# Optimization experiments

Measured on AMD Instinct MI355X. Metric: run time of the kernel, lower is better.

Reference implementation:

```python
import jax, jax.numpy as jnp
import numpy as np

NUM_COMPONENTS = 4
HEADS = 24
DIM_HEAD = 64
EPS = 1e-8

def setup_inputs() -> dict:
    key = jax.random.key(0)
    ks = jax.random.split(key, 6)
    BC, S, D = 8, 4096, 1536   # batch*components, spatial tokens, hidden dim
    T = 154                     # encoder (text) sequence length
    w_scale = D ** -0.5
    return {
        "hidden_states": jax.random.normal(ks[0], (BC, S, D), jnp.float32),
        "encoder_hidden_states": jax.random.normal(ks[1], (BC, T, D), jnp.float32),
        "Wq": jax.random.normal(ks[2], (D, D), jnp.float32) * w_scale,
        "bq": jnp.zeros((D,), jnp.float32),
        "Wk": jax.random.normal(ks[3], (D, D), jnp.float32) * w_scale,
        "bk": jnp.zeros((D,), jnp.float32),
        "Wv": jax.random.normal(ks[4], (D, D), jnp.float32) * w_scale,
        "bv": jnp.zeros((D,), jnp.float32),
        "Wo": jax.random.normal(ks[5], (D, D), jnp.float32) * w_scale,
        "bo": jnp.zeros((D,), jnp.float32),
    }

def reference(hidden_states, encoder_hidden_states, Wq, bq, Wk, bk, Wv, bv, Wo, bo):
    BC, S, D = hidden_states.shape
    T = encoder_hidden_states.shape[1]
    C = NUM_COMPONENTS
    B = BC // C
    H, dh = HEADS, DIM_HEAD
    scale = dh ** -0.5

    # linear projections (torch Linear: x @ W.T + b)
    q = hidden_states @ Wq.T + bq            # [BC, S, D]
    k = encoder_hidden_states @ Wk.T + bk     # [BC, T, D]
    v = encoder_hidden_states @ Wv.T + bv     # [BC, T, D]

    q = q.reshape(BC, S, H, dh).transpose(0, 2, 1, 3)  # [BC, H, S, dh]
    k = k.reshape(BC, T, H, dh).transpose(0, 2, 1, 3)  # [BC, H, T, dh]
    v = v.reshape(BC, T, H, dh).transpose(0, 2, 1, 3)  # [BC, H, T, dh]

    # full score tensor, softmax over the COMPONENT axis, then renormalize over keys
    scores = jnp.einsum('bhsd,bhtd->bhst', q, k) * scale        # [BC, H, S, T]
    scores = scores.reshape(C, B, H, S, T)
    w = jax.nn.softmax(scores, axis=0).reshape(BC, H, S, T)
    w = w / (jnp.sum(w, axis=-1, keepdims=True) + EPS)

    out = jnp.einsum('bhst,bhtd->bhsd', w, v)                   # [BC, H, S, dh]
    out = out.transpose(0, 2, 1, 3).reshape(BC, S, D)
    out = out @ Wo.T + bo
    return out
```

## Files before the change

### kernel.cpp

```cpp
#include <hip/hip_runtime.h>


typedef unsigned short u16;
typedef unsigned int   u32;

#define NHS   50331648ULL
#define NEHS  1892352ULL
#define NW    2359296ULL
#define NVT   1966080ULL

using bf16x8 = __attribute__((ext_vector_type(8))) short;
using f32x4  = __attribute__((ext_vector_type(4))) float;

__device__ __forceinline__ u16 f2bf(float f) {
  union { float f; u32 u; } x{f};
  u32 r = (x.u + 0x7fffu + ((x.u >> 16) & 1u)) >> 16;
  return (u16)r;
}

__device__ __forceinline__ void gload_lds16(const u16* g, u16* s) {
  __builtin_amdgcn_global_load_lds((const __attribute__((address_space(1))) void*)g,
                                   (__attribute__((address_space(3))) void*)s,
                                   16, 0, 0);
}

#define WAITV(N) asm volatile("s_waitcnt vmcnt(" #N ")" ::: "memory")

__global__ void cvt_bf16(const float* __restrict__ src, u16* __restrict__ dst, int n4) {
  int idx = blockIdx.x * blockDim.x + threadIdx.x;
  int stride = gridDim.x * blockDim.x;
  for (int i = idx; i < n4; i += stride) {
    float4 v = ((const float4*)src)[i];
    ushort4 o;
    o.x = f2bf(v.x); o.y = f2bf(v.y); o.z = f2bf(v.z); o.w = f2bf(v.w);
    ((ushort4*)dst)[i] = o;
  }
}

template <int MODE>
__global__ __launch_bounds__(512, 2)
void gemm_big(const u16* __restrict__ Ag, const u16* __restrict__ Bw,
              const float* __restrict__ bias, void* __restrict__ Cv) {
  __shared__ __align__(16) u16 lds[65536];

  const int tid  = threadIdx.x;
  const int wv   = tid >> 6;
  const int lane = tid & 63;
  const int l16  = lane & 15, quad = lane >> 4;
  const int wm = wv >> 2, wn = wv & 3;

  const int wg = ((int)blockIdx.x & 7) * 96 + ((int)blockIdx.x >> 3);
  const int by = wg & 127;
  const int bx = wg >> 7;
  const int m0 = by * 256, n0 = bx * 256;

  const u16* gsrc[4];
  int ldst[4];
#pragma unroll
  for (int q = 0; q < 4; ++q) {
    const int L = q * 512 + tid;
    const int cid = L & 1023;
    const int row = cid >> 2;
    const int csrc = ((L & 3) ^ ((row >> 1) & 3)) * 8;
    gsrc[q] = (L < 1024 ? Ag + (size_t)(m0 + row) * 1536
                        : Bw + (size_t)(n0 + row) * 1536) + csrc;
    ldst[q] = L * 8;
  }

  int aoff[8], boff[4];
#pragma unroll
  for (int i = 0; i < 8; ++i) {
    const int ra = wm * 128 + i * 16 + l16;
    aoff[i] = ra * 32 + ((quad ^ ((ra >> 1) & 3)) * 8);
  }
#pragma unroll
  for (int j = 0; j < 4; ++j) {
    const int rb = wn * 64 + j * 16 + l16;
    boff[j] = 8192 + rb * 32 + ((quad ^ ((rb >> 1) & 3)) * 8);
  }

  f32x4 acc[8][4];
#pragma unroll
  for (int i = 0; i < 8; ++i)
#pragma unroll
    for (int j = 0; j < 4; ++j) acc[i][j] = {0.f, 0.f, 0.f, 0.f};

  auto stage2 = [&](int tile, int qb) {
    u16* dst = &lds[(tile & 3) * 16384];
    const int kt = tile * 32;
    gload_lds16(gsrc[qb] + kt, dst + ldst[qb]);
    gload_lds16(gsrc[qb + 1] + kt, dst + ldst[qb + 1]);
  };

#define TILE_BODY(T, DO_STAGE, WAITCODE)                                      \
  {                                                                           \
    const u16* buf = &lds[((T) & 3) * 16384];                                 \
    bf16x8 bfr[4], af[4];                                                     \
    _Pragma("unroll") for (int j = 0; j < 4; ++j)                             \
      bfr[j] = *(const bf16x8*)&buf[boff[j]];                                 \
    _Pragma("unroll") for (int i = 0; i < 4; ++i)                             \
      af[i] = *(const bf16x8*)&buf[aoff[i]];                                  \
    if (DO_STAGE) stage2((T) + 3, 0);                                         \
    __builtin_amdgcn_s_barrier();                                             \
    __builtin_amdgcn_s_setprio(1);                                            \
    _Pragma("unroll") for (int i = 0; i < 4; ++i)                             \
      _Pragma("unroll") for (int j = 0; j < 4; ++j)                           \
        acc[i][j] = __builtin_amdgcn_mfma_f32_16x16x32_bf16(af[i], bfr[j],    \
                                                            acc[i][j], 0, 0, 0); \
    __builtin_amdgcn_s_setprio(0);                                            \
    __builtin_amdgcn_s_barrier();                                             \
    _Pragma("unroll") for (int i = 0; i < 4; ++i)                             \
      af[i] = *(const bf16x8*)&buf[aoff[4 + i]];                              \
    if (DO_STAGE) stage2((T) + 3, 2);                                         \
    __builtin_amdgcn_s_barrier();                                             \
    __builtin_amdgcn_s_setprio(1);                                            \
    _Pragma("unroll") for (int i = 0; i < 4; ++i)                             \
      _Pragma("unroll") for (int j = 0; j < 4; ++j)                           \
        acc[4 + i][j] = __builtin_amdgcn_mfma_f32_16x16x32_bf16(af[i], bfr[j],\
                                                        acc[4 + i][j], 0, 0, 0); \
    __builtin_amdgcn_s_setprio(0);                                            \
    WAITCODE;                                                                 \
    __builtin_amdgcn_s_barrier();                                             \
  }

  stage2(0, 0); stage2(0, 2);
  stage2(1, 0); stage2(1, 2);
  stage2(2, 0); stage2(2, 2);
  WAITV(8);
  __builtin_amdgcn_s_barrier();

  for (int t = 0; t < 45; ++t)
    TILE_BODY(t, true, WAITV(8));
  TILE_BODY(45, false, WAITV(4));
  TILE_BODY(46, false, WAITV(0));
  TILE_BODY(47, false, (void)0);
#undef TILE_BODY

#pragma unroll
  for (int i = 0; i < 8; ++i) {
    const int row0 = m0 + wm * 128 + i * 16 + quad * 4;
#pragma unroll
    for (int j = 0; j < 4; ++j) {
      const int col = n0 + wn * 64 + j * 16 + l16;
      const float bvs = bias[col];
#pragma unroll
      for (int rr = 0; rr < 4; ++rr) {
        const int row = row0 + rr;
        const float v = acc[i][j][rr] + bvs;
        if (MODE == 0) ((float*)Cv)[(size_t)row * 1536 + col] = v;
        else           ((u16*)Cv)[(size_t)row * 1536 + col] = f2bf(v);
      }
    }
  }
}

template <int MODE>
__global__ __launch_bounds__(256)
void gemm_bt(const u16* __restrict__ A, const u16* __restrict__ Bw,
             const float* __restrict__ bias, void* __restrict__ Cv,
             int M, int K) {
  const int N = 1536;
  __shared__ __align__(16) u16 As[4096];
  __shared__ __align__(16) u16 Bs[4096];
  const int tid  = threadIdx.x;
  const int wv   = tid >> 6;
  const int lane = tid & 63;
  const int wr = wv >> 1, wc = wv & 1;
  const int l16 = lane & 15, quad = lane >> 4;
  const int m0 = blockIdx.y * 128, n0 = blockIdx.x * 128;
  const int r = tid >> 2, c8 = (tid & 3) * 8;

  int ra0 = m0 + r;      if (ra0 > M - 1) ra0 = M - 1;
  int ra1 = m0 + 64 + r; if (ra1 > M - 1) ra1 = M - 1;
  const u16* a0 = A  + (size_t)ra0 * K + c8;
  const u16* a1 = A  + (size_t)ra1 * K + c8;
  const u16* b0 = Bw + (size_t)(n0 + r) * K + c8;
  const u16* b1 = Bw + (size_t)(n0 + 64 + r) * K + c8;
  u16* asd0 = &As[tid * 8];
  u16* asd1 = &As[2048 + tid * 8];
  u16* bsd0 = &Bs[tid * 8];
  u16* bsd1 = &Bs[2048 + tid * 8];

  f32x4 acc[4][4];
#pragma unroll
  for (int i = 0; i < 4; ++i)
#pragma unroll
    for (int j = 0; j < 4; ++j) acc[i][j] = {0.f, 0.f, 0.f, 0.f};

  for (int kt = 0; kt < K; kt += 32) {
    __syncthreads();
    gload_lds16(a0 + kt, asd0);
    gload_lds16(a1 + kt, asd1);
    gload_lds16(b0 + kt, bsd0);
    gload_lds16(b1 + kt, bsd1);
    __syncthreads();
    bf16x8 af[4], bfr[4];
#pragma unroll
    for (int i = 0; i < 4; ++i) {
      af[i]  = *(const bf16x8*)&As[(wr * 64 + i * 16 + l16) * 32 + quad * 8];
      bfr[i] = *(const bf16x8*)&Bs[(wc * 64 + i * 16 + l16) * 32 + quad * 8];
    }
#pragma unroll
    for (int i = 0; i < 4; ++i)
#pragma unroll
      for (int j = 0; j < 4; ++j)
        acc[i][j] = __builtin_amdgcn_mfma_f32_16x16x32_bf16(af[i], bfr[j], acc[i][j], 0, 0, 0);
  }

#pragma unroll
  for (int i = 0; i < 4; ++i) {
    const int rb = m0 + wr * 64 + i * 16 + quad * 4;
#pragma unroll
    for (int j = 0; j < 4; ++j) {
      const int col = n0 + wc * 64 + j * 16 + l16;
      const float bvs = bias[col];
#pragma unroll
      for (int rr = 0; rr < 4; ++rr) {
        const int row = rb + rr;
        if (row < M) {
          float v = acc[i][j][rr] + bvs;
          if (MODE == 1) {
            ((u16*)Cv)[(size_t)row * N + col] = f2bf(v);
          } else {
            const int bc = row / 154;
            const int t  = row - bc * 154;
            ((u16*)Cv)[((size_t)bc * 1536 + col) * 160 + t] = f2bf(v);
          }
        }
      }
    }
  }
}

__global__ __launch_bounds__(256, 2)
void attn_kernel(const u16* __restrict__ qg, const u16* __restrict__ kg,
                 const u16* __restrict__ vtg, u16* __restrict__ og) {
  __shared__ __align__(16) u16 lds[40960];

  const int tid  = threadIdx.x;
  const int wv   = tid >> 6;
  const int lane = tid & 63;
  const int l16 = lane & 15, quad = lane >> 4;
  const int s0 = blockIdx.x * 64;
  const int h  = blockIdx.y;
  const int b  = blockIdx.z;
  const int swz = ((quad ^ ((l16 >> 1) & 3)) * 8);

  {
    const u16* kbase = kg + (size_t)b * 154 * 1536 + h * 64;
#pragma unroll
    for (int p = 0; p < 20; ++p) {
      const int L = p * 256 + tid;
      const int r = L >> 2;
      const int t = r % 160;
      const int cks = r / 160;
      const int c = cks >> 1, ks = cks & 1;
      const int csrc = ((L & 3) ^ ((t >> 1) & 3)) * 8;
      const u16* src = kbase + ((size_t)c * 308 + t) * 1536 + ks * 32 + csrc;
      gload_lds16(src, &lds[(size_t)L * 8]);
    }
  }

  bf16x8 qa[4][2];
#pragma unroll
  for (int c = 0; c < 4; ++c) {
    const u16* qrow = qg + ((size_t)((c * 2 + b) * 4096 + s0 + wv * 16 + l16)) * 1536 + h * 64;
#pragma unroll
    for (int ks = 0; ks < 2; ++ks)
      qa[c][ks] = *(const bf16x8*)(qrow + ks * 32 + quad * 8);
  }
  __syncthreads();

  f32x4 sc[4][10];
#pragma unroll
  for (int c = 0; c < 4; ++c)
#pragma unroll
    for (int nt = 0; nt < 10; ++nt) sc[c][nt] = {0.f, 0.f, 0.f, 0.f};

#pragma unroll
  for (int nt = 0; nt < 10; ++nt)
#pragma unroll
    for (int c = 0; c < 4; ++c)
#pragma unroll
      for (int ks = 0; ks < 2; ++ks) {
        bf16x8 kf = *(const bf16x8*)&lds[((c * 2 + ks) * 160 + nt * 16 + l16) * 32 + swz];
        sc[c][nt] = __builtin_amdgcn_mfma_f32_16x16x32_bf16(qa[c][ks], kf, sc[c][nt], 0, 0, 0);
      }

  float rs[4][4];
#pragma unroll
  for (int c = 0; c < 4; ++c)
#pragma unroll
    for (int rr = 0; rr < 4; ++rr) rs[c][rr] = 0.f;

#pragma unroll
  for (int nt = 0; nt < 10; ++nt) {
    const int t = nt * 16 + l16;
    const bool ok = (t < 154);
#pragma unroll
    for (int rr = 0; rr < 4; ++rr) {
      float v0 = sc[0][nt][rr] * 0.125f;
      float v1 = sc[1][nt][rr] * 0.125f;
      float v2 = sc[2][nt][rr] * 0.125f;
      float v3 = sc[3][nt][rr] * 0.125f;
      float m = fmaxf(fmaxf(v0, v1), fmaxf(v2, v3));
      float e0 = __expf(v0 - m), e1 = __expf(v1 - m);
      float e2 = __expf(v2 - m), e3 = __expf(v3 - m);
      float inv = 1.f / (e0 + e1 + e2 + e3);
      float w0 = ok ? e0 * inv : 0.f;
      float w1 = ok ? e1 * inv : 0.f;
      float w2 = ok ? e2 * inv : 0.f;
      float w3 = ok ? e3 * inv : 0.f;
      sc[0][nt][rr] = w0; sc[1][nt][rr] = w1; sc[2][nt][rr] = w2; sc[3][nt][rr] = w3;
      rs[0][rr] += w0; rs[1][rr] += w1; rs[2][rr] += w2; rs[3][rr] += w3;
    }
  }
#pragma unroll
  for (int c = 0; c < 4; ++c)
#pragma unroll
    for (int rr = 0; rr < 4; ++rr) {
      float v = rs[c][rr];
      v += __shfl_xor(v, 1); v += __shfl_xor(v, 2);
      v += __shfl_xor(v, 4); v += __shfl_xor(v, 8);
      rs[c][rr] = 1.f / (v + 1e-8f);
    }

  __syncthreads();

  const u16* vbase = vtg + ((size_t)b * 1536 + h * 64) * 160;

  auto stage_v = [&](int c, int par) {
    const u16* vb = vbase + (size_t)c * 2 * 1536 * 160;
    u16* slot = &lds[20480 + par * 10240];
#pragma unroll
    for (int p = 0; p < 5; ++p) {
      const int L = p * 256 + tid;
      const int row = L >> 2;
      const int ks = row >> 6, dh = row & 63;
      const int csrc = ((L & 3) ^ ((dh >> 1) & 3)) * 8;
      gload_lds16(vb + dh * 160 + ks * 32 + csrc, &slot[(size_t)L * 8]);
    }
  };

  auto write_w = [&](int c, int par) {
    u16* slot = &lds[par * 10240];
#pragma unroll
    for (int nt = 0; nt < 10; ++nt) {
#pragma unroll
      for (int rr = 0; rr < 4; ++rr) {
        const int srow = wv * 16 + quad * 4 + rr;
        const int t = nt * 16 + l16;
        const int cl = ((t >> 3) & 3) ^ ((srow >> 1) & 3);
        slot[srow * 160 + (t >> 5) * 32 + cl * 8 + (t & 7)] =
            f2bf(sc[c][nt][rr] * rs[c][rr]);
      }
    }
  };

  f32x4 oacc[4][4];
#pragma unroll
  for (int c = 0; c < 4; ++c)
#pragma unroll
    for (int nd = 0; nd < 4; ++nd) oacc[c][nd] = {0.f, 0.f, 0.f, 0.f};

  stage_v(0, 0);
  write_w(0, 0);
#pragma unroll
  for (int c = 0; c < 4; ++c) {
    __syncthreads();
    if (c < 3) { stage_v(c + 1, (c + 1) & 1); write_w(c + 1, (c + 1) & 1); }
    const int par = c & 1;
    const u16* sw = &lds[par * 10240];
    const u16* sv = &lds[20480 + par * 10240];
#pragma unroll
    for (int ks = 0; ks < 5; ++ks) {
      bf16x8 wa = *(const bf16x8*)&sw[(wv * 16 + l16) * 160 + ks * 32 + swz];
#pragma unroll
      for (int nd = 0; nd < 4; ++nd) {
        bf16x8 vf = *(const bf16x8*)&sv[(ks * 64 + nd * 16 + l16) * 32 + swz];
        oacc[c][nd] = __builtin_amdgcn_mfma_f32_16x16x32_bf16(wa, vf, oacc[c][nd], 0, 0, 0);
      }
    }
  }

#pragma unroll
  for (int c = 0; c < 4; ++c)
#pragma unroll
    for (int nd = 0; nd < 4; ++nd)
#pragma unroll
      for (int rr = 0; rr < 4; ++rr) {
        const int srow = s0 + wv * 16 + quad * 4 + rr;
        og[((size_t)((c * 2 + b) * 4096 + srow)) * 1536 + h * 64 + nd * 16 + l16] =
            f2bf(oacc[c][nd][rr]);
      }
}

extern "C" void kernel_launch(void* const* d_in, const int* in_sizes, int n_in,
                              void* d_out, int out_size, void* d_ws, size_t ws_size,
                              hipStream_t stream) {
  (void)in_sizes; (void)n_in; (void)out_size; (void)ws_size;
  const float* hs  = (const float*)d_in[0];
  const float* ehs = (const float*)d_in[1];
  const float* Wq  = (const float*)d_in[2];
  const float* bq  = (const float*)d_in[3];
  const float* Wk  = (const float*)d_in[4];
  const float* bk  = (const float*)d_in[5];
  const float* Wv  = (const float*)d_in[6];
  const float* bv  = (const float*)d_in[7];
  const float* Wo  = (const float*)d_in[8];
  const float* bo  = (const float*)d_in[9];
  float* out = (float*)d_out;

  u16* ws   = (u16*)d_ws;
  u16* hsb  = ws;
  u16* ehsb = hsb + NHS;
  u16* wqb  = ehsb + NEHS;
  u16* wkb  = wqb + NW;
  u16* wvb  = wkb + NW;
  u16* wob  = wvb + NW;
  u16* qb   = wob + NW;
  u16* kgb  = qb + NHS;
  u16* vtb  = kgb + NEHS;
  u16* atb  = vtb + NVT;

  auto cvt = [&](const float* s, u16* d, size_t n) {
    int n4 = (int)(n / 4);
    int blocks = (n4 + 255) / 256;
    if (blocks > 8192) blocks = 8192;
    cvt_bf16<<<blocks, 256, 0, stream>>>(s, d, n4);
  };
  cvt(hs, hsb, NHS);
  cvt(ehs, ehsb, NEHS);
  cvt(Wq, wqb, NW);
  cvt(Wk, wkb, NW);
  cvt(Wv, wvb, NW);
  cvt(Wo, wob, NW);

  gemm_big<1><<<dim3(768), 512, 0, stream>>>(hsb, wqb, bq, qb);
  gemm_bt<1><<<dim3(12, 10), 256, 0, stream>>>(ehsb, wkb, bk, kgb, 1232, 1536);
  gemm_bt<2><<<dim3(12, 10), 256, 0, stream>>>(ehsb, wvb, bv, vtb, 1232, 1536);

  attn_kernel<<<dim3(64, 24, 2), 256, 0, stream>>>(qb, kgb, vtb, atb);

  gemm_big<0><<<dim3(768), 512, 0, stream>>>(atb, wob, bo, out);
}
```

Before: 904.1 us.

## Software-pipeline LDS fragment loads across tiles with register double buffering

```diff
diff --git a/kernel.cpp b/kernel.cpp
--- a/kernel.cpp
+++ b/kernel.cpp
@@ -25,6 +25,8 @@
 }
 
 #define WAITV(N) asm volatile("s_waitcnt vmcnt(" #N ")" ::: "memory")
+#define LGKM(N)  do { asm volatile("s_waitcnt lgkmcnt(" #N ")" ::: "memory"); \
+                      __builtin_amdgcn_sched_barrier(0); } while (0)
 
 __global__ void cvt_bf16(const float* __restrict__ src, u16* __restrict__ dst, int n4) {
   int idx = blockIdx.x * blockDim.x + threadIdx.x;
@@ -55,7 +57,6 @@
   const int m0 = by * 256, n0 = bx * 256;
 
   const u16* gsrc[4];
-  int ldst[4];
 #pragma unroll
   for (int q = 0; q < 4; ++q) {
     const int L = q * 512 + tid;
@@ -64,20 +65,13 @@
     const int csrc = ((L & 3) ^ ((row >> 1) & 3)) * 8;
     gsrc[q] = (L < 1024 ? Ag + (size_t)(m0 + row) * 1536
                         : Bw + (size_t)(n0 + row) * 1536) + csrc;
-    ldst[q] = L * 8;
-  }
-
-  int aoff[8], boff[4];
-#pragma unroll
-  for (int i = 0; i < 8; ++i) {
-    const int ra = wm * 128 + i * 16 + l16;
-    aoff[i] = ra * 32 + ((quad ^ ((ra >> 1) & 3)) * 8);
-  }
-#pragma unroll
-  for (int j = 0; j < 4; ++j) {
-    const int rb = wn * 64 + j * 16 + l16;
-    boff[j] = 8192 + rb * 32 + ((quad ^ ((rb >> 1) & 3)) * 8);
-  }
+  }
+  const int ldst0 = tid * 8;
+
+  const int ra = wm * 128 + l16;
+  const int aoff0 = ra * 32 + ((quad ^ ((ra >> 1) & 3)) * 8);
+  const int rb = wn * 64 + l16;
+  const int boff0 = 8192 + rb * 32 + ((quad ^ ((rb >> 1) & 3)) * 8);
 
   f32x4 acc[8][4];
 #pragma unroll
@@ -85,56 +79,78 @@
 #pragma unroll
     for (int j = 0; j < 4; ++j) acc[i][j] = {0.f, 0.f, 0.f, 0.f};
 
-  auto stage2 = [&](int tile, int qb) {
-    u16* dst = &lds[(tile & 3) * 16384];
+  auto stage4 = [&](int tile) {
+    u16* dst = &lds[(tile & 3) * 16384 + ldst0];
     const int kt = tile * 32;
-    gload_lds16(gsrc[qb] + kt, dst + ldst[qb]);
-    gload_lds16(gsrc[qb + 1] + kt, dst + ldst[qb + 1]);
+    gload_lds16(gsrc[0] + kt, dst);
+    gload_lds16(gsrc[1] + kt, dst + 4096);
+    gload_lds16(gsrc[2] + kt, dst + 8192);
+    gload_lds16(gsrc[3] + kt, dst + 12288);
   };
 
-#define TILE_BODY(T, DO_STAGE, WAITCODE)                                      \
-  {                                                                           \
-    const u16* buf = &lds[((T) & 3) * 16384];                                 \
-    bf16x8 bfr[4], af[4];                                                     \
+  bf16x8 afP[4], bfP[4], afQ[4], bfQ[4], afB[4];
+
+#define LOADSET(AF, BF, T) {                                                  \
+    const u16* u_ = &lds[((T) & 3) * 16384];                                  \
     _Pragma("unroll") for (int j = 0; j < 4; ++j)                             \
-      bfr[j] = *(const bf16x8*)&buf[boff[j]];                                 \
+      BF[j] = *(const bf16x8*)(u_ + boff0 + j * 512);                         \
     _Pragma("unroll") for (int i = 0; i < 4; ++i)                             \
-      af[i] = *(const bf16x8*)&buf[aoff[i]];                                  \
-    if (DO_STAGE) stage2((T) + 3, 0);                                         \
-    __builtin_amdgcn_s_barrier();                                             \
+      AF[i] = *(const bf16x8*)(u_ + aoff0 + i * 512);                         \
+  }
+#define LOADAFB(T) {                                                          \
+    const u16* u_ = &lds[((T) & 3) * 16384];                                  \
+    _Pragma("unroll") for (int i = 0; i < 4; ++i)                             \
+      afB[i] = *(const bf16x8*)(u_ + aoff0 + 2048 + i * 512);                 \
+  }
+#define MFMA16(AF, BF, BASE)                                                  \
     __builtin_amdgcn_s_setprio(1);                                            \
     _Pragma("unroll") for (int i = 0; i < 4; ++i)                             \
       _Pragma("unroll") for (int j = 0; j < 4; ++j)                           \
-        acc[i][j] = __builtin_amdgcn_mfma_f32_16x16x32_bf16(af[i], bfr[j],    \
-                                                            acc[i][j], 0, 0, 0); \
-    __builtin_amdgcn_s_setprio(0);                                            \
+        acc[(BASE) + i][j] = __builtin_amdgcn_mfma_f32_16x16x32_bf16(         \
+            AF[i], BF[j], acc[(BASE) + i][j], 0, 0, 0);                       \
+    __builtin_amdgcn_s_setprio(0)
+
+#define HALF1(T, AF, BF, DOSTAGE)                                             \
+    LOADAFB(T);                                                               \
+    if (DOSTAGE) stage4((T) + 3);                                             \
+    LGKM(4);                                                                  \
+    MFMA16(AF, BF, 0)
+#define HALF2(T, AFN, BFN, BFCUR, WCODE)                                      \
+    WCODE;                                                                    \
     __builtin_amdgcn_s_barrier();                                             \
-    _Pragma("unroll") for (int i = 0; i < 4; ++i)                             \
-      af[i] = *(const bf16x8*)&buf[aoff[4 + i]];                              \
-    if (DO_STAGE) stage2((T) + 3, 2);                                         \
-    __builtin_amdgcn_s_barrier();                                             \
-    __builtin_amdgcn_s_setprio(1);                                            \
-    _Pragma("unroll") for (int i = 0; i < 4; ++i)                             \
-      _Pragma("unroll") for (int j = 0; j < 4; ++j)                           \
-        acc[4 + i][j] = __builtin_amdgcn_mfma_f32_16x16x32_bf16(af[i], bfr[j],\
-                                                        acc[4 + i][j], 0, 0, 0); \
-    __builtin_amdgcn_s_setprio(0);                                            \
-    WAITCODE;                                                                 \
-    __builtin_amdgcn_s_barrier();                                             \
-  }
-
-  stage2(0, 0); stage2(0, 2);
-  stage2(1, 0); stage2(1, 2);
-  stage2(2, 0); stage2(2, 2);
+    LOADSET(AFN, BFN, (T) + 1);                                               \
+    LGKM(8);                                                                  \
+    MFMA16(afB, BFCUR, 4);                                                    \
+    __builtin_amdgcn_s_barrier()
+
+  stage4(0); stage4(1); stage4(2);
   WAITV(8);
   __builtin_amdgcn_s_barrier();
-
-  for (int t = 0; t < 45; ++t)
-    TILE_BODY(t, true, WAITV(8));
-  TILE_BODY(45, false, WAITV(4));
-  TILE_BODY(46, false, WAITV(0));
-  TILE_BODY(47, false, (void)0);
-#undef TILE_BODY
+  LOADSET(afP, bfP, 0);
+
+  for (int t = 0; t < 44; t += 2) {
+    HALF1(t, afP, bfP, true);
+    HALF2(t, afQ, bfQ, bfP, WAITV(8));
+    HALF1(t + 1, afQ, bfQ, true);
+    HALF2(t + 1, afP, bfP, bfQ, WAITV(8));
+  }
+  HALF1(44, afP, bfP, true);
+  HALF2(44, afQ, bfQ, bfP, WAITV(8));
+  HALF1(45, afQ, bfQ, false);
+  HALF2(45, afP, bfP, bfQ, WAITV(4));
+  HALF1(46, afP, bfP, false);
+  HALF2(46, afQ, bfQ, bfP, WAITV(0));
+  LOADAFB(47);
+  LGKM(4);
+  MFMA16(afQ, bfQ, 0);
+  LGKM(0);
+  MFMA16(afB, bfQ, 4);
+
+#undef HALF2
+#undef HALF1
+#undef MFMA16
+#undef LOADAFB
+#undef LOADSET
 
 #pragma unroll
   for (int i = 0; i < 8; ++i) {
```

Result: no change. 904.4 us (+0.0%).
